# Kernel tuning notes

Hardware: AMD Instinct MI355X
Metric: run time of the kernel (lower is better)

## Reference

```python
import jax, jax.numpy as jnp
import numpy as np

B, L, H, E, F, C = 8, 8192, 512, 8, 1024, 2  # batch, seq, hidden, experts, ffn, capacity factor


def setup_inputs() -> dict:
    key = jax.random.key(0)
    ks = jax.random.split(key, 4)
    x = jax.random.normal(ks[0], (B, L, H), jnp.float32)
    Wg = jax.random.normal(ks[1], (H, E), jnp.float32) * (H ** -0.5)   # gate (no bias)
    W1 = jax.random.normal(ks[2], (E, H, F), jnp.float32) * (H ** -0.5)
    b1 = jnp.zeros((E, F), jnp.float32)
    W2 = jax.random.normal(ks[3], (E, F, H), jnp.float32) * (F ** -0.5)
    b2 = jnp.zeros((E, H), jnp.float32)
    return {"x": x, "Wg": Wg, "W1": W1, "b1": b1, "W2": W2, "b2": b2}


def reference(x, Wg, W1, b1, W2, b2):
    b, l, h = x.shape
    e = Wg.shape[1]
    k = min(max(int(l * C / e), 1), l)  # expert-choice capacity per expert
    # Gate scores: softmax over experts per token, then each expert picks its top-k tokens.
    S = jax.nn.softmax(x @ Wg, axis=-1)          # (b, l, E)
    St = jnp.swapaxes(S, 1, 2)                   # (b, E, l)
    G, I = jax.lax.top_k(St, k)                  # (b, E, k) scores / token indices
    # Dispatch: gather each expert's chosen tokens.
    ex = jnp.take_along_axis(x[:, None], I[..., None], axis=2)   # (b, E, k, h)
    # Grouped expert MLP (Linear -> GELU -> Linear), batched over experts.
    hmid = jax.nn.gelu(jnp.einsum('bekh,ehf->bekf', ex, W1) + b1[None, :, None, :],
                       approximate=False)
    out = jnp.einsum('bekf,efh->bekh', hmid, W2) + b2[None, :, None, :]
    vals = G[..., None] * out                    # weight by gate score
    # Combine: scatter-add expert outputs back to token positions.
    new_x = jnp.zeros_like(x).at[jnp.arange(b)[:, None, None], I].add(vals)
    return new_x
```

## Files before the change

kernel.cpp:

```cpp
#include <hip/hip_runtime.h>
#include <hip/hip_bf16.h>
#include <hip/hip_fp16.h>

typedef float f32x4 __attribute__((ext_vector_type(4)));
typedef _Float16 f16x8 __attribute__((ext_vector_type(8)));

static constexpr int Bb = 8, Ll = 8192, Hh = 512, Ee = 8, Ff = 1024, KK = 2048;

static __device__ __forceinline__ float fast_rcp(float x) {
#if __has_builtin(__builtin_amdgcn_rcpf)
  return __builtin_amdgcn_rcpf(x);
#else
  return 1.0f / x;
#endif
}

static __device__ __forceinline__ float gelu_exact(float v) {
  float a = __builtin_fabsf(v) * 0.70710678118654752f;
  float t = fast_rcp(__builtin_fmaf(0.3275911f, a, 1.0f));
  float p = __builtin_fmaf(1.061405429f, t, -1.453152027f);
  p = __builtin_fmaf(p, t, 1.421413741f);
  p = __builtin_fmaf(p, t, -0.284496736f);
  p = __builtin_fmaf(p, t, 0.254829592f);
  p = p * t;
  float e = __expf(-a * a);
  float er = __builtin_fmaf(-p, e, 1.0f);
  er = __builtin_copysignf(er, v);
  return 0.5f * v * (1.0f + er);
}

__global__ __launch_bounds__(256) void transpose_cvt_kernel(const float* __restrict__ src,
                                                            _Float16* __restrict__ dst,
                                                            int R, int C) {
  __shared__ float tile[32][33];
  int z = blockIdx.z;
  const float* s = src + (size_t)z * R * C;
  _Float16* d = dst + (size_t)z * R * C;
  int c0 = blockIdx.x * 32, r0 = blockIdx.y * 32;
  int tx = threadIdx.x, ty = threadIdx.y;
#pragma unroll
  for (int i = ty; i < 32; i += 8) tile[i][tx] = s[(size_t)(r0 + i) * C + (c0 + tx)];
  __syncthreads();
#pragma unroll
  for (int i = ty; i < 32; i += 8) d[(size_t)(c0 + i) * R + (r0 + tx)] = (_Float16)tile[tx][i];
}

__global__ __launch_bounds__(256) void gatecvt_kernel(const float* __restrict__ x,
                                                      const float* __restrict__ Wg,
                                                      double* __restrict__ St,
                                                      _Float16* __restrict__ xb) {
  __shared__ float wgt[8][516];
  __shared__ float xs[32][68];
  int tid = threadIdx.x;
  for (int i = tid; i < Hh * Ee; i += 256) {
    int h = i >> 3, e = i & 7;
    wgt[e][h] = Wg[i];
  }
  int tl = tid >> 3, e = tid & 7;
  int token0 = blockIdx.x * 32;
  double acc = 0.0;
  for (int c = 0; c < 8; ++c) {
    __syncthreads();
#pragma unroll
    for (int i = tid; i < 512; i += 256) {
      int row = i >> 4, c4 = i & 15;
      float4 v = reinterpret_cast<const float4*>(x + (size_t)(token0 + row) * Hh + c * 64)[c4];
      *reinterpret_cast<float4*>(&xs[row][c4 * 4]) = v;
    }
    __syncthreads();
    {
      int row = tid >> 3, c8 = tid & 7;
      float4 v0 = *reinterpret_cast<const float4*>(&xs[row][c8 * 8]);
      float4 v1 = *reinterpret_cast<const float4*>(&xs[row][c8 * 8 + 4]);
      f16x8 h;
      h[0] = (_Float16)v0.x; h[1] = (_Float16)v0.y; h[2] = (_Float16)v0.z; h[3] = (_Float16)v0.w;
      h[4] = (_Float16)v1.x; h[5] = (_Float16)v1.y; h[6] = (_Float16)v1.z; h[7] = (_Float16)v1.w;
      *reinterpret_cast<f16x8*>(xb + (size_t)(token0 + row) * Hh + c * 64 + c8 * 8) = h;
    }
#pragma unroll
    for (int h = 0; h < 64; h += 4) {
      float4 xv = *reinterpret_cast<const float4*>(&xs[tl][h]);
      float4 wv = *reinterpret_cast<const float4*>(&wgt[e][c * 64 + h]);
      acc += (double)xv.x * (double)wv.x;
      acc += (double)xv.y * (double)wv.y;
      acc += (double)xv.z * (double)wv.z;
      acc += (double)xv.w * (double)wv.w;
    }
  }
  double m = acc;
  m = fmax(m, __shfl_xor(m, 1, 64));
  m = fmax(m, __shfl_xor(m, 2, 64));
  m = fmax(m, __shfl_xor(m, 4, 64));
  double ex = exp(acc - m);
  double s = ex;
  s += __shfl_xor(s, 1, 64);
  s += __shfl_xor(s, 2, 64);
  s += __shfl_xor(s, 4, 64);
  int token = token0 + tl;
  int b = token >> 13, l = token & (Ll - 1);
  St[((size_t)(b * Ee + e)) * Ll + l] = ex / s;
}

__global__ __launch_bounds__(1024) void topk_kernel(const double* __restrict__ St,
                                                    int* __restrict__ idx,
                                                    float* __restrict__ gate) {
  __shared__ unsigned long long keys[Ll];
  __shared__ unsigned int hist[256];
  __shared__ unsigned int sc[1024];
  __shared__ unsigned long long s_prefix;
  __shared__ int s_remaining;
  __shared__ unsigned long long redA[16], redO[16];
  int row = blockIdx.x;
  int tid = threadIdx.x;
  const double* s = St + (size_t)row * Ll;
  unsigned long long myA = ~0ULL, myO = 0ULL;
  for (int i = tid; i < Ll; i += 1024) {
    unsigned long long kx = (unsigned long long)__double_as_longlong(s[i]);
    keys[i] = kx;
    myA &= kx;
    myO |= kx;
  }
#pragma unroll
  for (int off2 = 32; off2 >= 1; off2 >>= 1) {
    myA &= __shfl_xor(myA, off2, 64);
    myO |= __shfl_xor(myO, off2, 64);
  }
  if ((tid & 63) == 0) { redA[tid >> 6] = myA; redO[tid >> 6] = myO; }
  __syncthreads();
  unsigned long long allA = redA[0], allO = redO[0];
#pragma unroll
  for (int w = 1; w < 16; ++w) { allA &= redA[w]; allO |= redO[w]; }
  unsigned long long diff = allA ^ allO;

  unsigned long long T;
  int nEqTake;
  if (diff == 0) {
    T = allA;
    nEqTake = KK;
  } else {
    int hb = 63 - __builtin_clzll(diff);
    int pv = hb >> 3;
    unsigned long long prefmask = (pv >= 7) ? 0ULL : (~0ULL << ((pv + 1) * 8));
    unsigned long long prefix = allA & prefmask;
    int remaining = KK;
    for (int p = pv; p >= 0; --p) {
      if (tid < 256) hist[tid] = 0;
      __syncthreads();
      int sh = p * 8;
      for (int i = tid; i < Ll; i += 1024) {
        unsigned long long kk = keys[i];
        if ((kk & prefmask) == prefix) atomicAdd(&hist[(unsigned)(kk >> sh) & 255u], 1u);
      }
      __syncthreads();
      if (tid < 256) sc[tid] = hist[tid];
      __syncthreads();
#pragma unroll
      for (int off = 1; off < 256; off <<= 1) {
        unsigned v = (tid < 256 && tid + off < 256) ? sc[tid + off] : 0;
        __syncthreads();
        if (tid < 256) sc[tid] += v;
        __syncthreads();
      }
      if (tid < 256) {
        unsigned incl = sc[tid];
        unsigned above = (tid == 255) ? 0u : sc[tid + 1];
        if ((int)incl >= remaining && (int)above < remaining) {
          s_remaining = remaining - (int)above;
          s_prefix = prefix | ((unsigned long long)(unsigned)tid << sh);
        }
      }
      __syncthreads();
      remaining = s_remaining;
      prefix = s_prefix;
      prefmask |= (255ULL << sh);
      __syncthreads();
    }
    T = prefix;
    nEqTake = remaining;
  }

  int base = tid * 8;
  unsigned long long kk[8];
  unsigned gtc = 0, eqc = 0;
#pragma unroll
  for (int j = 0; j < 8; ++j) {
    kk[j] = keys[base + j];
    gtc += (kk[j] > T);
    eqc += (kk[j] == T);
  }
  unsigned packed = (gtc << 16) | eqc;
  sc[tid] = packed;
  __syncthreads();
  for (int off = 1; off < 1024; off <<= 1) {
    unsigned v = (tid >= off) ? sc[tid - off] : 0;
    __syncthreads();
    sc[tid] += v;
    __syncthreads();
  }
  unsigned excl = sc[tid] - packed;
  int gtb = (int)(excl >> 16), eqb = (int)(excl & 0xFFFFu);
  int orow = row * KK;
#pragma unroll
  for (int j = 0; j < 8; ++j) {
    bool isgt = kk[j] > T, iseq = kk[j] == T;
    bool take = isgt || (iseq && eqb < nEqTake);
    if (take) {
      int pos = gtb + (eqb < nEqTake ? eqb : nEqTake);
      idx[orow + pos] = base + j;
      gate[orow + pos] = (float)__longlong_as_double((long long)kk[j]);
    }
    gtb += isgt ? 1 : 0;
    eqb += iseq ? 1 : 0;
  }
}

__global__ __launch_bounds__(256) void buildinv_kernel(const int* __restrict__ idx,
                                                       int* __restrict__ cnt,
                                                       int* __restrict__ inv) {
  int s = blockIdx.x * 256 + threadIdx.x;
  int gp = s >> 11;
  int b = gp >> 3;
  int t = idx[s];
  int key = b * Ll + t;
  int pos = atomicAdd(&cnt[key], 1);
  inv[key * 8 + pos] = s;
}

__global__ __launch_bounds__(256) void combine_kernel(const _Float16* __restrict__ yout,
                                                      const int* __restrict__ cnt,
                                                      const int* __restrict__ inv,
                                                      float* __restrict__ out) {
  int tglob = blockIdx.x * 4 + (threadIdx.x >> 6);
  int lane = threadIdx.x & 63;
  int n = cnt[tglob];
  float acc[8];
#pragma unroll
  for (int j = 0; j < 8; ++j) acc[j] = 0.f;
  for (int c = 0; c < n; ++c) {
    int s = inv[tglob * 8 + c];
    f16x8 v = *reinterpret_cast<const f16x8*>(yout + (size_t)s * Hh + lane * 8);
#pragma unroll
    for (int j = 0; j < 8; ++j) acc[j] += (float)v[j];
  }
  float* o = out + (size_t)tglob * Hh + lane * 8;
  f32x4 lo = {acc[0], acc[1], acc[2], acc[3]};
  f32x4 hi = {acc[4], acc[5], acc[6], acc[7]};
  *reinterpret_cast<f32x4*>(o) = lo;
  *reinterpret_cast<f32x4*>(o + 4) = hi;
}

__global__ __launch_bounds__(512, 2) void gemm1_kernel(const _Float16* __restrict__ xb,
                                                       const _Float16* __restrict__ w1t,
                                                       const float* __restrict__ b1,
                                                       const int* __restrict__ idx,
                                                       _Float16* __restrict__ hmid,
                                                       int chunk_base) {
  __shared__ __align__(16) _Float16 lds[65536];
  int tid = threadIdx.x, lane = tid & 63, wid = tid >> 6;
  int gp = chunk_base + blockIdx.z;
  int b = gp >> 3, e = gp & 7;
  int m0 = blockIdx.y * 256, f0 = blockIdx.x * 256;

  const _Float16* srcbase[8];
  int dstoff[8];
#pragma unroll
  for (int i = 0; i < 8; ++i) {
    int c = wid * 8 + i;
    int lr = (c & 31) * 8 + (lane >> 3);
    int q = lane & 7;
    int qg = q ^ (lr & 7);
    if (c < 32) {
      int token = idx[(size_t)gp * KK + m0 + lr];
      srcbase[i] = xb + ((size_t)b * Ll + token) * Hh + qg * 8;
      dstoff[i] = (c & 31) * 512;
    } else {
      srcbase[i] = w1t + ((size_t)e * Ff + f0 + lr) * Hh + qg * 8;
      dstoff[i] = 16384 + (c & 31) * 512;
    }
  }

  f32x4 acc[8][4] = {};
  int wm = wid >> 2, wn = wid & 3;
  int a_off[8], b_off[4];
  int ko = lane >> 4;
#pragma unroll
  for (int i = 0; i < 8; ++i) {
    int ra = wm * 128 + i * 16 + (lane & 15);
    a_off[i] = ra * 64 + (ko ^ (ra & 7)) * 8;
  }
#pragma unroll
  for (int i = 0; i < 4; ++i) {
    int rb = wn * 64 + i * 16 + (lane & 15);
    b_off[i] = 16384 + rb * 64 + (ko ^ (rb & 7)) * 8;
  }

  auto stage = [&](int p, int kt) {
#pragma unroll
    for (int i = 0; i < 8; ++i) {
      __builtin_amdgcn_global_load_lds(
          (const __attribute__((address_space(1))) void*)(srcbase[i] + kt),
          (__attribute__((address_space(3))) void*)(lds + p * 32768 + dstoff[i]), 16, 0, 0);
    }
  };

  constexpr int nt = Hh / 64;
  stage(0, 0);
  for (int t = 0; t < nt; ++t) {
    __syncthreads();
    if (t + 1 < nt) stage((t + 1) & 1, (t + 1) * 64);
    const _Float16* buf = lds + (t & 1) * 32768;
#pragma unroll
    for (int half = 0; half < 2; ++half) {
      int kx = half * 32;
      f16x8 af[8], bf[4];
#pragma unroll
      for (int i = 0; i < 8; ++i) af[i] = *reinterpret_cast<const f16x8*>(buf + (a_off[i] ^ kx));
#pragma unroll
      for (int i = 0; i < 4; ++i) bf[i] = *reinterpret_cast<const f16x8*>(buf + (b_off[i] ^ kx));
      __builtin_amdgcn_s_setprio(1);
#pragma unroll
      for (int fr = 0; fr < 8; ++fr)
#pragma unroll
        for (int fc = 0; fc < 4; ++fc)
          acc[fr][fc] = __builtin_amdgcn_mfma_f32_16x16x32_f16(af[fr], bf[fc], acc[fr][fc], 0, 0, 0);
      __builtin_amdgcn_s_setprio(0);
    }
  }
  __syncthreads();

  int cidx = lane & 15, rbase = (lane >> 4) * 4;
  float b1v[4];
#pragma unroll
  for (int fc = 0; fc < 4; ++fc) b1v[fc] = b1[e * Ff + f0 + wn * 64 + fc * 16 + cidx];
#pragma unroll
  for (int fr = 0; fr < 8; ++fr) {
#pragma unroll
    for (int fc = 0; fc < 4; ++fc) {
#pragma unroll
      for (int r = 0; r < 4; ++r) {
        int lm = wm * 128 + fr * 16 + rbase + r;
        int lf = wn * 64 + fc * 16 + cidx;
        float v = acc[fr][fc][r] + b1v[fc];
        float g = gelu_exact(v);
        lds[lm * 256 + (((lf >> 3) ^ (lm & 7)) << 3) + (lf & 7)] = (_Float16)g;
      }
    }
  }
  __syncthreads();
  _Float16* hd = hmid + (size_t)blockIdx.z * KK * Ff;
  int orow = tid >> 5, seg = tid & 31;
#pragma unroll
  for (int pp = 0; pp < 16; ++pp) {
    int lm = pp * 16 + orow;
    f16x8 v = *reinterpret_cast<const f16x8*>(lds + lm * 256 + ((seg ^ (lm & 7)) << 3));
    *reinterpret_cast<f16x8*>(hd + (size_t)(m0 + lm) * Ff + f0 + seg * 8) = v;
  }
}

__global__ __launch_bounds__(512, 2) void gemm2_kernel(const _Float16* __restrict__ hmid,
                                                       const _Float16* __restrict__ w2t,
                                                       const float* __restrict__ b2,
                                                       const int* __restrict__ idx,
                                                       const float* __restrict__ gate,
                                                       _Float16* __restrict__ yout,
                                                       int chunk_base) {
  __shared__ __align__(16) _Float16 lds[65536];
  int tid = threadIdx.x, lane = tid & 63, wid = tid >> 6;
  int gp = chunk_base + blockIdx.z;
  int e = gp & 7;
  int m0 = blockIdx.y * 256, h0 = blockIdx.x * 256;

  const _Float16* srcbase[8];
  int dstoff[8];
#pragma unroll
  for (int i = 0; i < 8; ++i) {
    int c = wid * 8 + i;
    int lr = (c & 31) * 8 + (lane >> 3);
    int q = lane & 7;
    int qg = q ^ (lr & 7);
    if (c < 32) {
      srcbase[i] = hmid + ((size_t)blockIdx.z * KK + m0 + lr) * Ff + qg * 8;
      dstoff[i] = (c & 31) * 512;
    } else {
      srcbase[i] = w2t + ((size_t)e * Hh + h0 + lr) * Ff + qg * 8;
      dstoff[i] = 16384 + (c & 31) * 512;
    }
  }

  f32x4 acc[8][4] = {};
  int wm = wid >> 2, wn = wid & 3;
  int a_off[8], b_off[4];
  int ko = lane >> 4;
#pragma unroll
  for (int i = 0; i < 8; ++i) {
    int ra = wm * 128 + i * 16 + (lane & 15);
    a_off[i] = ra * 64 + (ko ^ (ra & 7)) * 8;
  }
#pragma unroll
  for (int i = 0; i < 4; ++i) {
    int rb = wn * 64 + i * 16 + (lane & 15);
    b_off[i] = 16384 + rb * 64 + (ko ^ (rb & 7)) * 8;
  }

  auto stage = [&](int p, int kt) {
#pragma unroll
    for (int i = 0; i < 8; ++i) {
      __builtin_amdgcn_global_load_lds(
          (const __attribute__((address_space(1))) void*)(srcbase[i] + kt),
          (__attribute__((address_space(3))) void*)(lds + p * 32768 + dstoff[i]), 16, 0, 0);
    }
  };

  constexpr int nt = Ff / 64;
  stage(0, 0);
  for (int t = 0; t < nt; ++t) {
    __syncthreads();
    if (t + 1 < nt) stage((t + 1) & 1, (t + 1) * 64);
    const _Float16* buf = lds + (t & 1) * 32768;
#pragma unroll
    for (int half = 0; half < 2; ++half) {
      int kx = half * 32;
      f16x8 af[8], bf[4];
#pragma unroll
      for (int i = 0; i < 8; ++i) af[i] = *reinterpret_cast<const f16x8*>(buf + (a_off[i] ^ kx));
#pragma unroll
      for (int i = 0; i < 4; ++i) bf[i] = *reinterpret_cast<const f16x8*>(buf + (b_off[i] ^ kx));
      __builtin_amdgcn_s_setprio(1);
#pragma unroll
      for (int fr = 0; fr < 8; ++fr)
#pragma unroll
        for (int fc = 0; fc < 4; ++fc)
          acc[fr][fc] = __builtin_amdgcn_mfma_f32_16x16x32_f16(af[fr], bf[fc], acc[fr][fc], 0, 0, 0);
      __builtin_amdgcn_s_setprio(0);
    }
  }
  __syncthreads();

  int cidx = lane & 15, rbase = (lane >> 4) * 4;
  float b2v[4];
#pragma unroll
  for (int fc = 0; fc < 4; ++fc) b2v[fc] = b2[e * Hh + h0 + wn * 64 + fc * 16 + cidx];
#pragma unroll
  for (int fr = 0; fr < 8; ++fr) {
    float gv[4];
#pragma unroll
    for (int r = 0; r < 4; ++r) {
      int lm = wm * 128 + fr * 16 + rbase + r;
      gv[r] = gate[(size_t)gp * KK + m0 + lm];
    }
#pragma unroll
    for (int fc = 0; fc < 4; ++fc) {
#pragma unroll
      for (int r = 0; r < 4; ++r) {
        int lm = wm * 128 + fr * 16 + rbase + r;
        int lh = wn * 64 + fc * 16 + cidx;
        float v = acc[fr][fc][r] + b2v[fc];
        lds[lm * 256 + (((lh >> 3) ^ (lm & 7)) << 3) + (lh & 7)] = (_Float16)(gv[r] * v);
      }
    }
  }
  __syncthreads();
  int orow = tid >> 5, seg = tid & 31;
#pragma unroll
  for (int pp = 0; pp < 16; ++pp) {
    int lm = pp * 16 + orow;
    f16x8 v = *reinterpret_cast<const f16x8*>(lds + lm * 256 + ((seg ^ (lm & 7)) << 3));
    *reinterpret_cast<f16x8*>(yout + ((size_t)gp * KK + m0 + lm) * Hh + h0 + seg * 8) = v;
  }
}

extern "C" void kernel_launch(void* const* d_in, const int* in_sizes, int n_in,
                              void* d_out, int out_size, void* d_ws, size_t ws_size,
                              hipStream_t stream) {
  const float* x  = (const float*)d_in[0];
  const float* Wg = (const float*)d_in[1];
  const float* W1 = (const float*)d_in[2];
  const float* b1 = (const float*)d_in[3];
  const float* W2 = (const float*)d_in[4];
  const float* b2 = (const float*)d_in[5];
  float* out = (float*)d_out;

  char* ws = (char*)d_ws;
  size_t off = 0;
  auto alloc = [&](size_t bytes) -> char* {
    char* p = ws + off;
    off = (off + bytes + 255) & ~(size_t)255;
    return p;
  };
  _Float16* xb   = (_Float16*)alloc((size_t)Bb * Ll * Hh * 2);
  _Float16* w1t  = (_Float16*)alloc((size_t)Ee * Ff * Hh * 2);
  _Float16* w2t  = (_Float16*)alloc((size_t)Ee * Hh * Ff * 2);
  double*   St   = (double*)alloc((size_t)Bb * Ee * Ll * 8);
  int*      dI   = (int*)alloc((size_t)Bb * Ee * KK * 4);
  float*    dG   = (float*)alloc((size_t)Bb * Ee * KK * 4);
  int*      cnt  = (int*)alloc((size_t)Bb * Ll * 4);
  int*      inv  = (int*)alloc((size_t)Bb * Ll * 8 * 4);
  _Float16* yout = (_Float16*)alloc((size_t)Bb * Ee * KK * Hh * 2);
  size_t fixed = off;
  size_t per_pair = (size_t)KK * Ff * 2;
  int chunk = 1;
  if (fixed + per_pair * 16 <= ws_size) chunk = 16;
  else if (fixed + per_pair * 8 <= ws_size) chunk = 8;
  else if (fixed + per_pair * 4 <= ws_size) chunk = 4;
  else if (fixed + per_pair * 2 <= ws_size) chunk = 2;
  _Float16* hmid = (_Float16*)alloc(per_pair * (size_t)chunk);

  hipMemsetAsync(cnt, 0, (size_t)Bb * Ll * 4, stream);
  gatecvt_kernel<<<Bb * Ll / 32, 256, 0, stream>>>(x, Wg, St, xb);
  transpose_cvt_kernel<<<dim3(Ff / 32, Hh / 32, Ee), dim3(32, 8), 0, stream>>>(W1, w1t, Hh, Ff);
  transpose_cvt_kernel<<<dim3(Hh / 32, Ff / 32, Ee), dim3(32, 8), 0, stream>>>(W2, w2t, Ff, Hh);
  topk_kernel<<<Bb * Ee, 1024, 0, stream>>>(St, dI, dG);
  buildinv_kernel<<<Bb * Ee * KK / 256, 256, 0, stream>>>(dI, cnt, inv);

  for (int cb = 0; cb < Bb * Ee; cb += chunk) {
    gemm1_kernel<<<dim3(Ff / 256, KK / 256, chunk), 512, 0, stream>>>(xb, w1t, b1, dI, hmid, cb);
    gemm2_kernel<<<dim3(Hh / 256, KK / 256, chunk), 512, 0, stream>>>(hmid, w2t, b2, dI, dG, yout, cb);
  }
  combine_kernel<<<Bb * Ll / 4, 256, 0, stream>>>(yout, cnt, inv, out);
}
```

Before: 564.1 us.

## Remap GEMM grids to 1D with pair-interleaving, add nontemporal stores, streamline gate load

The GEMM launches now use a flat 1D grid. Blocks are decoded so that consecutive workgroups belong to different expert pairs, and gemm1 is split into two 256-block launches per 16-pair chunk, which changes how tiles spread across CUs and how caches are shared. Streaming outputs (xb, hmid, yout, the final output) and the yout loads in combine use nontemporal hints, to avoid polluting the cache with data that is not reused soon. The gate kernel now prefetches each x row directly into registers instead of staging a cooperative tile through LDS first. A nontemporal hint on hmid could hurt gemm2, which reads hmid back soon afterward. The fallback path also drops support for chunks smaller than 8.

```diff
diff --git a/kernel.cpp b/kernel.cpp
--- a/kernel.cpp
+++ b/kernel.cpp
@@ -4,6 +4,7 @@
 
 typedef float f32x4 __attribute__((ext_vector_type(4)));
 typedef _Float16 f16x8 __attribute__((ext_vector_type(8)));
+typedef unsigned int u32x4 __attribute__((ext_vector_type(4)));
 
 static constexpr int Bb = 8, Ll = 8192, Hh = 512, Ee = 8, Ff = 1024, KK = 2048;
 
@@ -29,6 +30,11 @@
   return 0.5f * v * (1.0f + er);
 }
 
+static __device__ __forceinline__ void nt_store16(const f16x8& v, _Float16* p) {
+  __builtin_nontemporal_store(*reinterpret_cast<const u32x4*>(&v),
+                              reinterpret_cast<u32x4*>(p));
+}
+
 __global__ __launch_bounds__(256) void transpose_cvt_kernel(const float* __restrict__ src,
                                                             _Float16* __restrict__ dst,
                                                             int R, int C) {
@@ -52,35 +58,32 @@
   __shared__ float wgt[8][516];
   __shared__ float xs[32][68];
   int tid = threadIdx.x;
-  for (int i = tid; i < Hh * Ee; i += 256) {
-    int h = i >> 3, e = i & 7;
-    wgt[e][h] = Wg[i];
-  }
-  int tl = tid >> 3, e = tid & 7;
+  for (int i = tid; i < Hh * Ee; i += 256) wgt[i & 7][i >> 3] = Wg[i];
+  int row = tid >> 3, seg = tid & 7;
+  int tl = row, e = seg;
   int token0 = blockIdx.x * 32;
+  const float* xrow = x + (size_t)(token0 + row) * Hh;
+  _Float16* xbrow = xb + (size_t)(token0 + row) * Hh;
+  float4 r0 = reinterpret_cast<const float4*>(xrow)[seg * 2];
+  float4 r1 = reinterpret_cast<const float4*>(xrow)[seg * 2 + 1];
   double acc = 0.0;
   for (int c = 0; c < 8; ++c) {
+    f16x8 h;
+    h[0] = (_Float16)r0.x; h[1] = (_Float16)r0.y; h[2] = (_Float16)r0.z; h[3] = (_Float16)r0.w;
+    h[4] = (_Float16)r1.x; h[5] = (_Float16)r1.y; h[6] = (_Float16)r1.z; h[7] = (_Float16)r1.w;
+    nt_store16(h, xbrow + c * 64 + seg * 8);
     __syncthreads();
-#pragma unroll
-    for (int i = tid; i < 512; i += 256) {
-      int row = i >> 4, c4 = i & 15;
-      float4 v = reinterpret_cast<const float4*>(x + (size_t)(token0 + row) * Hh + c * 64)[c4];
-      *reinterpret_cast<float4*>(&xs[row][c4 * 4]) = v;
+    *reinterpret_cast<float4*>(&xs[row][seg * 8]) = r0;
+    *reinterpret_cast<float4*>(&xs[row][seg * 8 + 4]) = r1;
+    if (c + 1 < 8) {
+      r0 = reinterpret_cast<const float4*>(xrow + (c + 1) * 64)[seg * 2];
+      r1 = reinterpret_cast<const float4*>(xrow + (c + 1) * 64)[seg * 2 + 1];
     }
     __syncthreads();
-    {
-      int row = tid >> 3, c8 = tid & 7;
-      float4 v0 = *reinterpret_cast<const float4*>(&xs[row][c8 * 8]);
-      float4 v1 = *reinterpret_cast<const float4*>(&xs[row][c8 * 8 + 4]);
-      f16x8 h;
-      h[0] = (_Float16)v0.x; h[1] = (_Float16)v0.y; h[2] = (_Float16)v0.z; h[3] = (_Float16)v0.w;
-      h[4] = (_Float16)v1.x; h[5] = (_Float16)v1.y; h[6] = (_Float16)v1.z; h[7] = (_Float16)v1.w;
-      *reinterpret_cast<f16x8*>(xb + (size_t)(token0 + row) * Hh + c * 64 + c8 * 8) = h;
-    }
-#pragma unroll
-    for (int h = 0; h < 64; h += 4) {
-      float4 xv = *reinterpret_cast<const float4*>(&xs[tl][h]);
-      float4 wv = *reinterpret_cast<const float4*>(&wgt[e][c * 64 + h]);
+#pragma unroll
+    for (int hh = 0; hh < 64; hh += 4) {
+      float4 xv = *reinterpret_cast<const float4*>(&xs[tl][hh]);
+      float4 wv = *reinterpret_cast<const float4*>(&wgt[e][c * 64 + hh]);
       acc += (double)xv.x * (double)wv.x;
       acc += (double)xv.y * (double)wv.y;
       acc += (double)xv.z * (double)wv.z;
@@ -238,15 +241,17 @@
   for (int j = 0; j < 8; ++j) acc[j] = 0.f;
   for (int c = 0; c < n; ++c) {
     int s = inv[tglob * 8 + c];
-    f16x8 v = *reinterpret_cast<const f16x8*>(yout + (size_t)s * Hh + lane * 8);
+    u32x4 u = __builtin_nontemporal_load(
+        reinterpret_cast<const u32x4*>(yout + (size_t)s * Hh + lane * 8));
+    f16x8 v = *reinterpret_cast<f16x8*>(&u);
 #pragma unroll
     for (int j = 0; j < 8; ++j) acc[j] += (float)v[j];
   }
   float* o = out + (size_t)tglob * Hh + lane * 8;
   f32x4 lo = {acc[0], acc[1], acc[2], acc[3]};
   f32x4 hi = {acc[4], acc[5], acc[6], acc[7]};
-  *reinterpret_cast<f32x4*>(o) = lo;
-  *reinterpret_cast<f32x4*>(o + 4) = hi;
+  __builtin_nontemporal_store(lo, reinterpret_cast<f32x4*>(o));
+  __builtin_nontemporal_store(hi, reinterpret_cast<f32x4*>(o + 4));
 }
 
 __global__ __launch_bounds__(512, 2) void gemm1_kernel(const _Float16* __restrict__ xb,
@@ -254,12 +259,17 @@
                                                        const float* __restrict__ b1,
                                                        const int* __restrict__ idx,
                                                        _Float16* __restrict__ hmid,
-                                                       int chunk_base) {
+                                                       int chunk_base, int slotbase) {
   __shared__ __align__(16) _Float16 lds[65536];
   int tid = threadIdx.x, lane = tid & 63, wid = tid >> 6;
-  int gp = chunk_base + blockIdx.z;
+  int nat = blockIdx.x;
+  int zz = nat & 7;
+  int rem = nat >> 3;
+  int bx = rem & 3, by = rem >> 2;
+  int gp = chunk_base + zz;
+  int slot = slotbase + zz;
   int b = gp >> 3, e = gp & 7;
-  int m0 = blockIdx.y * 256, f0 = blockIdx.x * 256;
+  int m0 = by * 256, f0 = bx * 256;
 
   const _Float16* srcbase[8];
   int dstoff[8];
@@ -341,19 +351,18 @@
         int lm = wm * 128 + fr * 16 + rbase + r;
         int lf = wn * 64 + fc * 16 + cidx;
         float v = acc[fr][fc][r] + b1v[fc];
-        float g = gelu_exact(v);
-        lds[lm * 256 + (((lf >> 3) ^ (lm & 7)) << 3) + (lf & 7)] = (_Float16)g;
+        lds[lm * 256 + (((lf >> 3) ^ (lm & 7)) << 3) + (lf & 7)] = (_Float16)gelu_exact(v);
       }
     }
   }
   __syncthreads();
-  _Float16* hd = hmid + (size_t)blockIdx.z * KK * Ff;
+  _Float16* hd = hmid + (size_t)slot * KK * Ff;
   int orow = tid >> 5, seg = tid & 31;
 #pragma unroll
   for (int pp = 0; pp < 16; ++pp) {
     int lm = pp * 16 + orow;
     f16x8 v = *reinterpret_cast<const f16x8*>(lds + lm * 256 + ((seg ^ (lm & 7)) << 3));
-    *reinterpret_cast<f16x8*>(hd + (size_t)(m0 + lm) * Ff + f0 + seg * 8) = v;
+    nt_store16(v, hd + (size_t)(m0 + lm) * Ff + f0 + seg * 8);
   }
 }
 
@@ -363,12 +372,23 @@
                                                        const int* __restrict__ idx,
                                                        const float* __restrict__ gate,
                                                        _Float16* __restrict__ yout,
-                                                       int chunk_base) {
+                                                       int chunk_base, int pairs16) {
   __shared__ __align__(16) _Float16 lds[65536];
   int tid = threadIdx.x, lane = tid & 63, wid = tid >> 6;
-  int gp = chunk_base + blockIdx.z;
+  int nat = blockIdx.x;
+  int zz, rem;
+  if (pairs16) {
+    zz = (nat & 7) * 2 + ((nat >> 3) & 1);
+    rem = nat >> 4;
+  } else {
+    zz = nat & 7;
+    rem = nat >> 3;
+  }
+  int bx = rem & 1, by = rem >> 1;
+  int gp = chunk_base + zz;
+  int slot = zz;
   int e = gp & 7;
-  int m0 = blockIdx.y * 256, h0 = blockIdx.x * 256;
+  int m0 = by * 256, h0 = bx * 256;
 
   const _Float16* srcbase[8];
   int dstoff[8];
@@ -379,7 +399,7 @@
     int q = lane & 7;
     int qg = q ^ (lr & 7);
     if (c < 32) {
-      srcbase[i] = hmid + ((size_t)blockIdx.z * KK + m0 + lr) * Ff + qg * 8;
+      srcbase[i] = hmid + ((size_t)slot * KK + m0 + lr) * Ff + qg * 8;
       dstoff[i] = (c & 31) * 512;
     } else {
       srcbase[i] = w2t + ((size_t)e * Hh + h0 + lr) * Ff + qg * 8;
@@ -465,7 +485,7 @@
   for (int pp = 0; pp < 16; ++pp) {
     int lm = pp * 16 + orow;
     f16x8 v = *reinterpret_cast<const f16x8*>(lds + lm * 256 + ((seg ^ (lm & 7)) << 3));
-    *reinterpret_cast<f16x8*>(yout + ((size_t)gp * KK + m0 + lm) * Hh + h0 + seg * 8) = v;
+    nt_store16(v, yout + ((size_t)gp * KK + m0 + lm) * Hh + h0 + seg * 8);
   }
 }
 
@@ -498,11 +518,8 @@
   _Float16* yout = (_Float16*)alloc((size_t)Bb * Ee * KK * Hh * 2);
   size_t fixed = off;
   size_t per_pair = (size_t)KK * Ff * 2;
-  int chunk = 1;
-  if (fixed + per_pair * 16 <= ws_size) chunk = 16;
-  else if (fixed + per_pair * 8 <= ws_size) chunk = 8;
-  else if (fixed + per_pair * 4 <= ws_size) chunk = 4;
-  else if (fixed + per_pair * 2 <= ws_size) chunk = 2;
+  bool big = (fixed + per_pair * 16 <= ws_size);
+  int chunk = big ? 16 : 8;
   _Float16* hmid = (_Float16*)alloc(per_pair * (size_t)chunk);
 
   hipMemsetAsync(cnt, 0, (size_t)Bb * Ll * 4, stream);
@@ -512,9 +529,17 @@
   topk_kernel<<<Bb * Ee, 1024, 0, stream>>>(St, dI, dG);
   buildinv_kernel<<<Bb * Ee * KK / 256, 256, 0, stream>>>(dI, cnt, inv);
 
-  for (int cb = 0; cb < Bb * Ee; cb += chunk) {
-    gemm1_kernel<<<dim3(Ff / 256, KK / 256, chunk), 512, 0, stream>>>(xb, w1t, b1, dI, hmid, cb);
-    gemm2_kernel<<<dim3(Hh / 256, KK / 256, chunk), 512, 0, stream>>>(hmid, w2t, b2, dI, dG, yout, cb);
+  if (big) {
+    for (int cb = 0; cb < Bb * Ee; cb += 16) {
+      gemm1_kernel<<<256, 512, 0, stream>>>(xb, w1t, b1, dI, hmid, cb, 0);
+      gemm1_kernel<<<256, 512, 0, stream>>>(xb, w1t, b1, dI, hmid, cb + 8, 8);
+      gemm2_kernel<<<256, 512, 0, stream>>>(hmid, w2t, b2, dI, dG, yout, cb, 1);
+    }
+  } else {
+    for (int cb = 0; cb < Bb * Ee; cb += 8) {
+      gemm1_kernel<<<256, 512, 0, stream>>>(xb, w1t, b1, dI, hmid, cb, 0);
+      gemm2_kernel<<<128, 512, 0, stream>>>(hmid, w2t, b2, dI, dG, yout, cb, 0);
+    }
   }
   combine_kernel<<<Bb * Ll / 4, 256, 0, stream>>>(yout, cnt, inv, out);
 }
```

Result: faster. 543.5 us (-3.6%).
